# Kernel optimization log

Measured on AMD Instinct MI355X. Metric: run time of the kernel, lower is better.

## Reference

```python
import jax, jax.numpy as jnp
import numpy as np

B, S, DIM = 2, 1024, 2048
H, NOPE, ROPE_D, VD = 16, 128, 64, 128
QKD = NOPE + ROPE_D  # 192
BASE = 10000
NEG_INF = -1e9


def _rope_cos_sin(seq_len, start_pos=0):
    # theta: [ROPE_D//2]
    theta = 1.0 / (BASE ** (jnp.arange(0, ROPE_D, 2, dtype=jnp.float32) / ROPE_D))
    pos = jnp.arange(start_pos, start_pos + seq_len, dtype=jnp.float32)
    ang = pos[:, None] * theta[None, :]  # [s, ROPE_D//2]
    return jnp.cos(ang), jnp.sin(ang)


def _apply_rope(x, cos, sin):
    # x: [b, s, h, d]; cos/sin: [s, d//2]
    b, s, h, d = x.shape
    xs = x.astype(jnp.float32).reshape(b, s, h, d // 2, 2)
    c = cos[None, :, None, :]
    sn = sin[None, :, None, :]
    out = jnp.stack([xs[..., 0] * c - xs[..., 1] * sn,
                     xs[..., 1] * c + xs[..., 0] * sn], axis=-1)
    return out.reshape(b, s, h, d).astype(x.dtype)


def setup_inputs() -> dict:
    key = jax.random.key(0)
    ks = jax.random.split(key, 6)
    x = jax.random.normal(ks[0], (B, S, DIM), dtype=jnp.float32)
    sc = lambda fan_in: 1.0 / np.sqrt(fan_in)
    Wq = jax.random.normal(ks[1], (DIM, H * QKD), dtype=jnp.float32) * sc(DIM)
    Wk = jax.random.normal(ks[2], (DIM, H * QKD), dtype=jnp.float32) * sc(DIM)
    Wv = jax.random.normal(ks[3], (DIM, H * VD), dtype=jnp.float32) * sc(DIM)
    Wo = jax.random.normal(ks[4], (H * VD, DIM), dtype=jnp.float32) * sc(H * VD)
    bo = jnp.zeros((DIM,), dtype=jnp.float32)
    mask = jnp.where(jnp.tril(jnp.ones((S, S), dtype=bool)), 0.0, NEG_INF).astype(jnp.float32)
    return {"x": x, "Wq": Wq, "Wk": Wk, "Wv": Wv, "Wo": Wo, "bo": bo,
            "mask": mask, "start_pos": 0}


def reference(x, Wq, Wk, Wv, Wo, bo, mask, start_pos):
    b, s, _ = x.shape
    q = (x @ Wq).reshape(b, s, H, QKD)
    k = (x @ Wk).reshape(b, s, H, QKD)
    v = (x @ Wv).reshape(b, s, H, VD)
    q_nope, q_rope = q[..., :NOPE], q[..., NOPE:]
    k_nope, k_rope = k[..., :NOPE], k[..., NOPE:]
    cos, sin = _rope_cos_sin(s)  # input_pos=None -> positions 0..s-1
    q_rope = _apply_rope(q_rope, cos, sin)
    k_rope = _apply_rope(k_rope, cos, sin)
    q = jnp.concatenate([q_nope, q_rope], axis=-1)
    k = jnp.concatenate([k_nope, k_rope], axis=-1)
    # start_pos=0 prefill: cache[:end_pos] == k, v just written
    scale = QKD ** -0.5
    scores = jnp.einsum('bshd,bthd->bsht', q, k) * scale
    scores = scores + mask[:, None, :]  # mask.unsqueeze(1) on [b,s,h,t] broadcasting
    weights = jax.nn.softmax(scores.astype(jnp.float32), axis=-1).astype(x.dtype)
    c_v = jnp.einsum('bsht,bthd->bshd', weights, v)
    return c_v.reshape(b, s, H * VD) @ Wo + bo
```

## Files before the change

kernel.cpp:

```cpp
#include <hip/hip_runtime.h>


typedef __bf16 bf16;
typedef __bf16 bf16x8 __attribute__((ext_vector_type(8)));
typedef __bf16 bf16x4 __attribute__((ext_vector_type(4)));
typedef float  f32x4  __attribute__((ext_vector_type(4)));

#define DEVI __device__ __forceinline__

static constexpr int Bc = 2, Sc = 1024, DIMc = 2048, Hc = 16;
static constexpr int NOPEc = 128, QKDc = 192, VDc = 128;
static constexpr int NQ    = Hc * QKDc;
static constexpr int NCAT  = NQ + NQ + Hc*VDc;

__global__ __launch_bounds__(256) void k_prep(const float* __restrict__ x,
                                              const float* __restrict__ Wq, const float* __restrict__ Wk,
                                              const float* __restrict__ Wv, const float* __restrict__ Wo,
                                              bf16* __restrict__ xb, bf16* __restrict__ wcat,
                                              bf16* __restrict__ woT,
                                              float* __restrict__ cosT, float* __restrict__ sinT) {
    __shared__ float tile[64][68];
    const int yt = blockIdx.y, xt = blockIdx.x, tid = threadIdx.x;
    if (yt < 160) {
        const float* src; bf16* dst; int N, n0;
        if (yt < 48)       { src = Wq; N = 3072; n0 = yt * 64;         dst = wcat; }
        else if (yt < 96)  { src = Wk; N = 3072; n0 = (yt - 48) * 64;  dst = wcat + (size_t)3072 * 2048; }
        else if (yt < 128) { src = Wv; N = 2048; n0 = (yt - 96) * 64;  dst = wcat + (size_t)6144 * 2048; }
        else               { src = Wo; N = 2048; n0 = (yt - 128) * 64; dst = woT; }
        int k0 = xt * 64;
        int tr = tid >> 4, tc = (tid & 15) * 4;
#pragma unroll
        for (int i = 0; i < 4; i++) {
            int r = tr + i * 16;
            float4 v = *(const float4*)(src + (size_t)(k0 + r) * N + n0 + tc);
            tile[r][tc+0] = v.x; tile[r][tc+1] = v.y; tile[r][tc+2] = v.z; tile[r][tc+3] = v.w;
        }
        __syncthreads();
#pragma unroll
        for (int i = 0; i < 4; i++) {
            int n = tr + i * 16;
            bf16x4 o;
#pragma unroll
            for (int j = 0; j < 4; j++) o[j] = (bf16)tile[tc + j][n];
            *(bf16x4*)(dst + (size_t)(n0 + n) * 2048 + k0 + tc) = o;
        }
    } else if (yt < 224) {
        int i = (((yt - 160) * 32 + xt) * 256 + tid) * 8;
        float4 a = *(const float4*)(x + i);
        float4 b = *(const float4*)(x + i + 4);
        bf16x8 o;
        o[0]=(bf16)a.x; o[1]=(bf16)a.y; o[2]=(bf16)a.z; o[3]=(bf16)a.w;
        o[4]=(bf16)b.x; o[5]=(bf16)b.y; o[6]=(bf16)b.z; o[7]=(bf16)b.w;
        *(bf16x8*)(xb + i) = o;
    } else {
#pragma unroll
        for (int p = 0; p < 4; p++) {
            int idx = p * 8192 + xt * 256 + tid;
            int pos = idx >> 5, i = idx & 31;
            float theta = expf(-(float)i * (9.210340371976184f / 32.0f));
            float ang = (float)pos * theta;
            cosT[idx] = cosf(ang);
            sinT[idx] = sinf(ang);
        }
    }
}

__global__ __launch_bounds__(256) void k_rope2(bf16* __restrict__ qkv, const float* __restrict__ cosT,
                                               const float* __restrict__ sinT) {
    int bidx = blockIdx.x;
    int secbase = (bidx >= 1024) ? NQ : 0;
    int idx = (bidx & 1023) * 256 + threadIdx.x;
    int g = idx & 7, h = (idx >> 3) & 15, row = idx >> 7;
    int s = row & (Sc - 1);
    bf16* p = qkv + (size_t)row * NCAT + secbase + h * QKDc + NOPEc + g * 8;
    bf16x8 v = *(bf16x8*)p;
    const float* cp = cosT + s * 32 + g * 4;
    const float* sp = sinT + s * 32 + g * 4;
#pragma unroll
    for (int q = 0; q < 4; q++) {
        float x0 = (float)v[2*q], x1 = (float)v[2*q+1];
        float c = cp[q], sn = sp[q];
        v[2*q]   = (bf16)(x0 * c - x1 * sn);
        v[2*q+1] = (bf16)(x1 * c + x0 * sn);
    }
    *(bf16x8*)p = v;
}

__global__ __launch_bounds__(256) void k_vt(const bf16* __restrict__ qkv, bf16* __restrict__ vT) {
    int st = blockIdx.x, dt = blockIdx.y, bh = blockIdx.z;
    int b = bh >> 4, h = bh & 15;
    __shared__ bf16 tile[64][72];
    int r = threadIdx.x >> 3, c8 = (threadIdx.x & 7) * 8;
    const bf16* src = qkv + (size_t)(b * Sc + st * 64) * NCAT + 2 * NQ + h * VDc + dt * 64;
#pragma unroll
    for (int i = 0; i < 2; i++) {
        int rr = r + i * 32;
        *(bf16x8*)&tile[rr][c8] = *(const bf16x8*)(src + (size_t)rr * NCAT + c8);
    }
    __syncthreads();
    bf16* dst = vT + ((size_t)bh * 128 + dt * 64) * Sc + st * 64;
#pragma unroll
    for (int i = 0; i < 2; i++) {
        int rr = r + i * 32;
        bf16x8 o;
#pragma unroll
        for (int j = 0; j < 8; j++) o[j] = tile[c8 + j][rr];
        *(bf16x8*)(dst + (size_t)rr * Sc + c8) = o;
    }
}

DEVI void gload16(const bf16* g, bf16* l) {
    __builtin_amdgcn_global_load_lds((const __attribute__((address_space(1))) void*)g,
                                     (__attribute__((address_space(3))) void*)l, 16, 0, 0);
}

__global__ __launch_bounds__(512, 2) void k_gemm8(const bf16* __restrict__ A, const bf16* __restrict__ Bt,
                                                  bf16* __restrict__ C, int N, int K, int NCT) {
    __shared__ __align__(16) bf16 lds[2][2][2][256 * 32];
    const int tid = threadIdx.x;
    const int l = tid & 63, wid = tid >> 6;
    const int lg = l >> 4, lc = l & 15;
    const int wm = wid >> 2, wn = wid & 3;
    const int bid = blockIdx.x;
    const int xcd = bid & 7, g = bid >> 3;
    const int per = NCT >> 3;
    const int rt = g & 7, ct = xcd * per + (g >> 3);
    const int row0 = rt * 256, col0 = ct * 256;
    const int NT = K >> 6;

    const bf16* Abase = A  + (size_t)row0 * K;
    const bf16* Bbase = Bt + (size_t)col0 * K;

    size_t srcoff0, srcoff1;
    int ldsoff0, ldsoff1;
    {
        int li0 = tid,        r0 = li0 >> 2, u0 = li0 & 3;
        int li1 = 512 + tid,  r1 = li1 >> 2, u1 = li1 & 3;
        srcoff0 = (size_t)r0 * K + ((u0 ^ ((r0 >> 1) & 3)) << 3);  ldsoff0 = li0 * 8;
        srcoff1 = (size_t)r1 * K + ((u1 ^ ((r1 >> 1) & 3)) << 3);  ldsoff1 = li1 * 8;
    }

#define STAGE8(ab, ks, ktile, buf) { \
    const bf16* gb_ = ((ab) ? Bbase : Abase) + (ktile) * 64 + (ks) * 32; \
    bf16* lb_ = &lds[buf][ab][ks][0]; \
    gload16(gb_ + srcoff0, lb_ + ldsoff0); \
    gload16(gb_ + srcoff1, lb_ + ldsoff1); }

    f32x4 acc[8][4] = {};

    STAGE8(0, 0, 0, 0); STAGE8(1, 0, 0, 0); STAGE8(0, 1, 0, 0); STAGE8(1, 1, 0, 0);
    asm volatile("s_waitcnt vmcnt(4)" ::: "memory");
    __builtin_amdgcn_s_barrier();
    asm volatile("" ::: "memory");

    for (int kt = 0; kt < NT; ++kt) {
        const int cur = kt & 1, nxt = cur ^ 1;
        const bool notlast = (kt + 1 < NT);
        bf16x8 aF[4], bB[4];
#pragma unroll
        for (int ph = 0; ph < 4; ph++) {
            const int ks = ph >> 1, mh = ph & 1;
            const bf16* As_ = &lds[cur][0][ks][0];
            const bf16* Bs_ = &lds[cur][1][ks][0];
            if (mh == 0) {
#pragma unroll
                for (int fc = 0; fc < 4; fc++) {
                    int row = wn * 64 + fc * 16 + lc;
                    bB[fc] = *(const bf16x8*)(Bs_ + row * 32 + ((lg ^ ((row >> 1) & 3)) << 3));
                }
            }
#pragma unroll
            for (int i = 0; i < 4; i++) {
                int row = wm * 128 + (mh * 4 + i) * 16 + lc;
                aF[i] = *(const bf16x8*)(As_ + row * 32 + ((lg ^ ((row >> 1) & 3)) << 3));
            }
            if (notlast) {
                if      (ph == 0) STAGE8(0, 0, kt + 1, nxt)
                else if (ph == 1) STAGE8(1, 0, kt + 1, nxt)
                else if (ph == 2) STAGE8(0, 1, kt + 1, nxt)
                else              STAGE8(1, 1, kt + 1, nxt)
            }
            __builtin_amdgcn_s_barrier();
            asm volatile("" ::: "memory");
            __builtin_amdgcn_s_setprio(1);
#pragma unroll
            for (int i = 0; i < 4; i++)
#pragma unroll
                for (int fc = 0; fc < 4; fc++)
                    acc[mh * 4 + i][fc] =
                        __builtin_amdgcn_mfma_f32_16x16x32_bf16(aF[i], bB[fc], acc[mh * 4 + i][fc], 0, 0, 0);
            __builtin_amdgcn_s_setprio(0);
            if (ph == 1) {
                if (notlast) asm volatile("s_waitcnt vmcnt(4)" ::: "memory");
                else         asm volatile("s_waitcnt vmcnt(0)" ::: "memory");
            }
            if (ph == 3 && notlast) {
                asm volatile("s_waitcnt vmcnt(4)" ::: "memory");
            }
            __builtin_amdgcn_s_barrier();
            asm volatile("" ::: "memory");
        }
    }
#undef STAGE8
#pragma unroll
    for (int m = 0; m < 8; m++)
#pragma unroll
        for (int fc = 0; fc < 4; fc++)
#pragma unroll
            for (int j = 0; j < 4; j++) {
                int r = row0 + wm * 128 + m * 16 + lg * 4 + j;
                int c = col0 + wn * 64 + fc * 16 + lc;
                C[(size_t)r * N + c] = (bf16)acc[m][fc][j];
            }
}

__global__ __launch_bounds__(512, 2) void k_gemmO(const bf16* __restrict__ A, const bf16* __restrict__ Bt,
                                                  float* __restrict__ C, const float* __restrict__ bias,
                                                  int N, int K) {
    __shared__ __align__(16) bf16 lds[2][2][2][128 * 32];
    const int tid = threadIdx.x;
    const int l = tid & 63, wid = tid >> 6;
    const int lg = l >> 4, lc = l & 15;
    const int wm = wid >> 2, wn = wid & 3;
    const int bid = blockIdx.x;
    const int xcd = bid & 7, g = bid >> 3;
    const int rt = g & 15, ct = xcd * 2 + (g >> 4);
    const int row0 = rt * 128, col0 = ct * 128;
    const int NT = K >> 6;

    const bf16* Abase = A  + (size_t)row0 * K;
    const bf16* Bbase = Bt + (size_t)col0 * K;

    size_t srcoff; int ldsoff;
    {
        int r0 = tid >> 2, u0 = tid & 3;
        srcoff = (size_t)r0 * K + ((u0 ^ ((r0 >> 1) & 3)) << 3);
        ldsoff = tid * 8;
    }

#define STAGEO(ab, ks, ktile, buf) { \
    const bf16* gb_ = ((ab) ? Bbase : Abase) + (ktile) * 64 + (ks) * 32; \
    gload16(gb_ + srcoff, &lds[buf][ab][ks][0] + ldsoff); }

    f32x4 acc[4][2] = {};

    STAGEO(0, 0, 0, 0); STAGEO(1, 0, 0, 0); STAGEO(0, 1, 0, 0); STAGEO(1, 1, 0, 0);
    asm volatile("s_waitcnt vmcnt(2)" ::: "memory");
    __builtin_amdgcn_s_barrier();
    asm volatile("" ::: "memory");

    for (int kt = 0; kt < NT; ++kt) {
        const int cur = kt & 1, nxt = cur ^ 1;
        const bool notlast = (kt + 1 < NT);
#pragma unroll
        for (int ph = 0; ph < 2; ph++) {
            const bf16* As_ = &lds[cur][0][ph][0];
            const bf16* Bs_ = &lds[cur][1][ph][0];
            bf16x8 aF[4], bB[2];
#pragma unroll
            for (int n = 0; n < 2; n++) {
                int row = wn * 32 + n * 16 + lc;
                bB[n] = *(const bf16x8*)(Bs_ + row * 32 + ((lg ^ ((row >> 1) & 3)) << 3));
            }
#pragma unroll
            for (int m = 0; m < 4; m++) {
                int row = wm * 64 + m * 16 + lc;
                aF[m] = *(const bf16x8*)(As_ + row * 32 + ((lg ^ ((row >> 1) & 3)) << 3));
            }
            if (notlast) {
                if (ph == 0) { STAGEO(0, 0, kt + 1, nxt); STAGEO(1, 0, kt + 1, nxt); }
                else         { STAGEO(0, 1, kt + 1, nxt); STAGEO(1, 1, kt + 1, nxt); }
            }
            __builtin_amdgcn_s_barrier();
            asm volatile("" ::: "memory");
            __builtin_amdgcn_s_setprio(1);
#pragma unroll
            for (int m = 0; m < 4; m++)
#pragma unroll
                for (int n = 0; n < 2; n++)
                    acc[m][n] = __builtin_amdgcn_mfma_f32_16x16x32_bf16(aF[m], bB[n], acc[m][n], 0, 0, 0);
            __builtin_amdgcn_s_setprio(0);
            if (notlast)          asm volatile("s_waitcnt vmcnt(2)" ::: "memory");
            else if (ph == 0)     asm volatile("s_waitcnt vmcnt(0)" ::: "memory");
            __builtin_amdgcn_s_barrier();
            asm volatile("" ::: "memory");
        }
    }
#undef STAGEO
#pragma unroll
    for (int m = 0; m < 4; m++)
#pragma unroll
        for (int n = 0; n < 2; n++)
#pragma unroll
            for (int j = 0; j < 4; j++) {
                int r = row0 + wm * 64 + m * 16 + lg * 4 + j;
                int c = col0 + wn * 32 + n * 16 + lc;
                C[(size_t)r * N + c] = acc[m][n][j] + bias[c];
            }
}

__global__ __launch_bounds__(256, 3) void k_attn(const bf16* __restrict__ qkv, const bf16* __restrict__ vT,
                                                 bf16* __restrict__ cv) {
    const int bid = blockIdx.x;
    const int xcd = bid & 7, g = bid >> 3;
    const int qt = (g & 32) ? (g & 15) : (15 - (g & 15));
    const int bh = xcd + 8 * (g >> 4);
    const int b = bh >> 4, h = bh & 15;
    const int tid = threadIdx.x, l = tid & 63, w = tid >> 6;
    const int lg = l >> 4, lc = l & 15;
    __shared__ __align__(16) bf16 Ks[64 * 192];
    __shared__ __align__(16) bf16 Vs[128 * 64];
    __shared__ __align__(16) bf16 Pl[4][16][72];
    const bf16* Qb = qkv + (size_t)b * Sc * NCAT + h * QKDc;
    const bf16* Kb = Qb + NQ;
    const bf16* Vt = vT + (size_t)bh * 128 * Sc;

    int sK[6];
#pragma unroll
    for (int r = 0; r < 6; r++) {
        int li = r * 256 + tid;
        int row = li / 24, c16 = li - row * 24;
        sK[r] = row * NCAT + ((c16 ^ (row & 7)) * 8);
    }
    int sV[4];
#pragma unroll
    for (int r = 0; r < 4; r++) {
        int li = r * 256 + tid;
        int row = li >> 3, c16 = li & 7;
        sV[r] = row * Sc + ((c16 ^ (row & 7)) * 8);
    }
    const int swz = lc & 7;

    bf16x8 qF[6];
    const int qrow = qt * 64 + w * 16 + lc;
#pragma unroll
    for (int kc = 0; kc < 6; kc++) qF[kc] = *(const bf16x8*)(Qb + (size_t)qrow * NCAT + kc * 32 + lg * 8);

    f32x4 acc[8] = {};
    float mrow[4] = {-1e30f, -1e30f, -1e30f, -1e30f};
    float lsum[4] = {0.f, 0.f, 0.f, 0.f};
    const float scale = 0.07216878364870323f;

#pragma unroll
    for (int r = 0; r < 6; r++) gload16(Kb + sK[r], Ks + (r * 256 + tid) * 8);

    for (int c = 0; c <= qt; ++c) {
        const int t0 = c * 64;
        __syncthreads();
#pragma unroll
        for (int r = 0; r < 4; r++) gload16(Vt + t0 + sV[r], Vs + (r * 256 + tid) * 8);
        f32x4 sc[4] = {};
#pragma unroll
        for (int nt = 0; nt < 4; nt++)
#pragma unroll
            for (int kc = 0; kc < 6; kc++) {
                bf16x8 kf = *(const bf16x8*)(Ks + (nt * 16 + lc) * 192 + (((kc * 4 + lg) ^ swz) * 8));
                sc[nt] = __builtin_amdgcn_mfma_f32_16x16x32_bf16(qF[kc], kf, sc[nt], 0, 0, 0);
            }
        __syncthreads();
        if (c < qt) {
#pragma unroll
            for (int r = 0; r < 6; r++) gload16(Kb + (size_t)(t0 + 64) * NCAT + sK[r], Ks + (r * 256 + tid) * 8);
        }
        float p[4][4];
        float cmax[4] = {-1e30f, -1e30f, -1e30f, -1e30f};
        const bool diag = (c == qt);
#pragma unroll
        for (int nt = 0; nt < 4; nt++)
#pragma unroll
            for (int j = 0; j < 4; j++) {
                float v = sc[nt][j] * scale;
                if (diag) {
                    int tg = t0 + nt * 16 + lc;
                    int rg = qt * 64 + w * 16 + lg * 4 + j;
                    if (tg > rg) v = -1e9f;
                }
                p[nt][j] = v;
                cmax[j] = fmaxf(cmax[j], v);
            }
#pragma unroll
        for (int j = 0; j < 4; j++)
#pragma unroll
            for (int d = 1; d < 16; d <<= 1) cmax[j] = fmaxf(cmax[j], __shfl_xor(cmax[j], d));
        float f[4];
#pragma unroll
        for (int j = 0; j < 4; j++) {
            float nm = fmaxf(mrow[j], cmax[j]);
            f[j] = __expf(mrow[j] - nm);
            mrow[j] = nm;
        }
        float psum[4] = {0.f, 0.f, 0.f, 0.f};
#pragma unroll
        for (int nt = 0; nt < 4; nt++)
#pragma unroll
            for (int j = 0; j < 4; j++) {
                p[nt][j] = __expf(p[nt][j] - mrow[j]);
                psum[j] += p[nt][j];
            }
#pragma unroll
        for (int j = 0; j < 4; j++) {
#pragma unroll
            for (int d = 1; d < 16; d <<= 1) psum[j] += __shfl_xor(psum[j], d);
            lsum[j] = lsum[j] * f[j] + psum[j];
        }
#pragma unroll
        for (int n = 0; n < 8; n++)
#pragma unroll
            for (int j = 0; j < 4; j++) acc[n][j] *= f[j];
#pragma unroll
        for (int nt = 0; nt < 4; nt++)
#pragma unroll
            for (int j = 0; j < 4; j++)
                Pl[w][lg * 4 + j][nt * 16 + lc] = (bf16)p[nt][j];
#pragma unroll
        for (int ks = 0; ks < 2; ks++) {
            bf16x8 aP = *(const bf16x8*)(&Pl[w][lc][ks * 32 + lg * 8]);
#pragma unroll
            for (int n = 0; n < 8; n++) {
                bf16x8 bV = *(const bf16x8*)(Vs + (n * 16 + lc) * 64 + (((ks * 4 + lg) ^ swz) * 8));
                acc[n] = __builtin_amdgcn_mfma_f32_16x16x32_bf16(aP, bV, acc[n], 0, 0, 0);
            }
        }
    }
#pragma unroll
    for (int j = 0; j < 4; j++) {
        float inv = 1.0f / lsum[j];
        int r = qt * 64 + w * 16 + lg * 4 + j;
#pragma unroll
        for (int n = 0; n < 8; n++) {
            float v = acc[n][j] * inv;
            cv[((size_t)(b * Sc + r) * Hc + h) * VDc + n * 16 + lc] = (bf16)v;
        }
    }
}

extern "C" void kernel_launch(void* const* d_in, const int* in_sizes, int n_in,
                              void* d_out, int out_size, void* d_ws, size_t ws_size,
                              hipStream_t stream) {
    const float* x  = (const float*)d_in[0];
    const float* Wq = (const float*)d_in[1];
    const float* Wk = (const float*)d_in[2];
    const float* Wv = (const float*)d_in[3];
    const float* Wo = (const float*)d_in[4];
    const float* bo = (const float*)d_in[5];
    float* out = (float*)d_out;
    char* ws = (char*)d_ws;

    bf16*  wcat = (bf16*)(ws + 0);
    bf16*  woT  = (bf16*)(ws + 33554432);
    bf16*  xb   = (bf16*)(ws + 41943040);
    bf16*  qkvb = (bf16*)(ws + 50331648);
    bf16*  cvb  = (bf16*)(ws + 83886080);
    bf16*  vTb  = (bf16*)(ws + 92274688);
    float* cosT = (float*)(ws + 100663296);
    float* sinT = (float*)(ws + 100794368);

    k_prep<<<dim3(32, 225), 256, 0, stream>>>(x, Wq, Wk, Wv, Wo, xb, wcat, woT, cosT, sinT);
    k_gemm8<<<256, 512, 0, stream>>>(xb, wcat, qkvb, NCAT, DIMc, NCAT / 256);
    k_rope2<<<2048, 256, 0, stream>>>(qkvb, cosT, sinT);
    k_vt<<<dim3(16, 2, 32), 256, 0, stream>>>(qkvb, vTb);
    k_attn<<<512, 256, 0, stream>>>(qkvb, vTb, cvb);
    k_gemmO<<<256, 512, 0, stream>>>(cvb, woT, out, bo, DIMc, DIMc);
}
```

Before: 163.9 us.

## Software-pipeline LDS fragment reads ahead of MFMA phases in QKV GEMM

Result: no change. 163.9 us (-0.0%).

```diff
diff --git a/kernel.cpp b/kernel.cpp
--- a/kernel.cpp
+++ b/kernel.cpp
@@ -146,62 +146,73 @@
     gload16(gb_ + srcoff0, lb_ + ldsoff0); \
     gload16(gb_ + srcoff1, lb_ + ldsoff1); }
 
+#define RD_A(dst, P, hf) { _Pragma("unroll") \
+    for (int i_ = 0; i_ < 4; i_++) { \
+        int row_ = wm * 128 + ((hf) * 4 + i_) * 16 + lc; \
+        dst[i_] = *(const bf16x8*)((P) + row_ * 32 + ((lg ^ ((row_ >> 1) & 3)) << 3)); } }
+#define RD_B(dst, P) { _Pragma("unroll") \
+    for (int fc_ = 0; fc_ < 4; fc_++) { \
+        int row_ = wn * 64 + fc_ * 16 + lc; \
+        dst[fc_] = *(const bf16x8*)((P) + row_ * 32 + ((lg ^ ((row_ >> 1) & 3)) << 3)); } }
+#define MM(Av, Bv, mo) { _Pragma("unroll") \
+    for (int i_ = 0; i_ < 4; i_++) _Pragma("unroll") \
+        for (int fc_ = 0; fc_ < 4; fc_++) \
+            acc[(mo) + i_][fc_] = __builtin_amdgcn_mfma_f32_16x16x32_bf16(Av[i_], Bv[fc_], acc[(mo) + i_][fc_], 0, 0, 0); }
+#define BAR() { __builtin_amdgcn_s_barrier(); asm volatile("" ::: "memory"); }
+
     f32x4 acc[8][4] = {};
 
     STAGE8(0, 0, 0, 0); STAGE8(1, 0, 0, 0); STAGE8(0, 1, 0, 0); STAGE8(1, 1, 0, 0);
     asm volatile("s_waitcnt vmcnt(4)" ::: "memory");
-    __builtin_amdgcn_s_barrier();
-    asm volatile("" ::: "memory");
+    BAR();
 
     for (int kt = 0; kt < NT; ++kt) {
         const int cur = kt & 1, nxt = cur ^ 1;
         const bool notlast = (kt + 1 < NT);
-        bf16x8 aF[4], bB[4];
-#pragma unroll
-        for (int ph = 0; ph < 4; ph++) {
-            const int ks = ph >> 1, mh = ph & 1;
-            const bf16* As_ = &lds[cur][0][ks][0];
-            const bf16* Bs_ = &lds[cur][1][ks][0];
-            if (mh == 0) {
-#pragma unroll
-                for (int fc = 0; fc < 4; fc++) {
-                    int row = wn * 64 + fc * 16 + lc;
-                    bB[fc] = *(const bf16x8*)(Bs_ + row * 32 + ((lg ^ ((row >> 1) & 3)) << 3));
-                }
-            }
-#pragma unroll
-            for (int i = 0; i < 4; i++) {
-                int row = wm * 128 + (mh * 4 + i) * 16 + lc;
-                aF[i] = *(const bf16x8*)(As_ + row * 32 + ((lg ^ ((row >> 1) & 3)) << 3));
-            }
-            if (notlast) {
-                if      (ph == 0) STAGE8(0, 0, kt + 1, nxt)
-                else if (ph == 1) STAGE8(1, 0, kt + 1, nxt)
-                else if (ph == 2) STAGE8(0, 1, kt + 1, nxt)
-                else              STAGE8(1, 1, kt + 1, nxt)
-            }
-            __builtin_amdgcn_s_barrier();
-            asm volatile("" ::: "memory");
-            __builtin_amdgcn_s_setprio(1);
-#pragma unroll
-            for (int i = 0; i < 4; i++)
-#pragma unroll
-                for (int fc = 0; fc < 4; fc++)
-                    acc[mh * 4 + i][fc] =
-                        __builtin_amdgcn_mfma_f32_16x16x32_bf16(aF[i], bB[fc], acc[mh * 4 + i][fc], 0, 0, 0);
-            __builtin_amdgcn_s_setprio(0);
-            if (ph == 1) {
-                if (notlast) asm volatile("s_waitcnt vmcnt(4)" ::: "memory");
-                else         asm volatile("s_waitcnt vmcnt(0)" ::: "memory");
-            }
-            if (ph == 3 && notlast) {
-                asm volatile("s_waitcnt vmcnt(4)" ::: "memory");
-            }
-            __builtin_amdgcn_s_barrier();
-            asm volatile("" ::: "memory");
-        }
+        const bf16* A0_ = &lds[cur][0][0][0];
+        const bf16* A1_ = &lds[cur][0][1][0];
+        const bf16* B0_ = &lds[cur][1][0][0];
+        const bf16* B1_ = &lds[cur][1][1][0];
+        bf16x8 aX[4], aY[4], bX[4], bY[4];
+        RD_A(aX, A0_, 0);
+        RD_B(bX, B0_);
+        if (notlast) STAGE8(0, 0, kt + 1, nxt);
+        RD_A(aY, A0_, 1);
+        BAR();
+        __builtin_amdgcn_s_setprio(1);
+        MM(aX, bX, 0);
+        __builtin_amdgcn_s_setprio(0);
+        if (notlast) asm volatile("s_waitcnt vmcnt(2)" ::: "memory");
+        else         asm volatile("s_waitcnt vmcnt(0)" ::: "memory");
+        BAR();
+        if (notlast) STAGE8(1, 0, kt + 1, nxt);
+        RD_A(aX, A1_, 0);
+        RD_B(bY, B1_);
+        BAR();
+        __builtin_amdgcn_s_setprio(1);
+        MM(aY, bX, 4);
+        __builtin_amdgcn_s_setprio(0);
+        BAR();
+        if (notlast) STAGE8(0, 1, kt + 1, nxt);
+        RD_A(aY, A1_, 1);
+        BAR();
+        __builtin_amdgcn_s_setprio(1);
+        MM(aX, bY, 0);
+        __builtin_amdgcn_s_setprio(0);
+        BAR();
+        if (notlast) STAGE8(1, 1, kt + 1, nxt);
+        BAR();
+        __builtin_amdgcn_s_setprio(1);
+        MM(aY, bY, 4);
+        __builtin_amdgcn_s_setprio(0);
+        if (notlast) asm volatile("s_waitcnt vmcnt(4)" ::: "memory");
+        BAR();
     }
 #undef STAGE8
+#undef RD_A
+#undef RD_B
+#undef MM
+#undef BAR
 #pragma unroll
     for (int m = 0; m < 8; m++)
 #pragma unroll
```

## Shrink QKV GEMM tile to 256x128 with single-phase K=32 loop; fuse rope and V-transpose

Applied to the files above, without the earlier changes.

Measured after the change: 166.9 us. About the same (+1.8%).

```diff
diff --git a/kernel.cpp b/kernel.cpp
--- a/kernel.cpp
+++ b/kernel.cpp
@@ -65,47 +65,48 @@
     }
 }
 
-__global__ __launch_bounds__(256) void k_rope2(bf16* __restrict__ qkv, const float* __restrict__ cosT,
-                                               const float* __restrict__ sinT) {
-    int bidx = blockIdx.x;
-    int secbase = (bidx >= 1024) ? NQ : 0;
-    int idx = (bidx & 1023) * 256 + threadIdx.x;
-    int g = idx & 7, h = (idx >> 3) & 15, row = idx >> 7;
-    int s = row & (Sc - 1);
-    bf16* p = qkv + (size_t)row * NCAT + secbase + h * QKDc + NOPEc + g * 8;
-    bf16x8 v = *(bf16x8*)p;
-    const float* cp = cosT + s * 32 + g * 4;
-    const float* sp = sinT + s * 32 + g * 4;
-#pragma unroll
-    for (int q = 0; q < 4; q++) {
-        float x0 = (float)v[2*q], x1 = (float)v[2*q+1];
-        float c = cp[q], sn = sp[q];
-        v[2*q]   = (bf16)(x0 * c - x1 * sn);
-        v[2*q+1] = (bf16)(x1 * c + x0 * sn);
-    }
-    *(bf16x8*)p = v;
-}
-
-__global__ __launch_bounds__(256) void k_vt(const bf16* __restrict__ qkv, bf16* __restrict__ vT) {
-    int st = blockIdx.x, dt = blockIdx.y, bh = blockIdx.z;
-    int b = bh >> 4, h = bh & 15;
-    __shared__ bf16 tile[64][72];
-    int r = threadIdx.x >> 3, c8 = (threadIdx.x & 7) * 8;
-    const bf16* src = qkv + (size_t)(b * Sc + st * 64) * NCAT + 2 * NQ + h * VDc + dt * 64;
-#pragma unroll
-    for (int i = 0; i < 2; i++) {
-        int rr = r + i * 32;
-        *(bf16x8*)&tile[rr][c8] = *(const bf16x8*)(src + (size_t)rr * NCAT + c8);
-    }
-    __syncthreads();
-    bf16* dst = vT + ((size_t)bh * 128 + dt * 64) * Sc + st * 64;
-#pragma unroll
-    for (int i = 0; i < 2; i++) {
-        int rr = r + i * 32;
-        bf16x8 o;
-#pragma unroll
-        for (int j = 0; j < 8; j++) o[j] = tile[c8 + j][rr];
-        *(bf16x8*)(dst + (size_t)rr * Sc + c8) = o;
+__global__ __launch_bounds__(256) void k_ropevt(bf16* __restrict__ qkv, const float* __restrict__ cosT,
+                                                const float* __restrict__ sinT, bf16* __restrict__ vT) {
+    const int bidx = blockIdx.x, tid = threadIdx.x;
+    if (bidx < 2048) {
+        int secbase = (bidx >= 1024) ? NQ : 0;
+        int idx = (bidx & 1023) * 256 + tid;
+        int g = idx & 7, h = (idx >> 3) & 15, row = idx >> 7;
+        int s = row & (Sc - 1);
+        bf16* p = qkv + (size_t)row * NCAT + secbase + h * QKDc + NOPEc + g * 8;
+        bf16x8 v = *(bf16x8*)p;
+        const float* cp = cosT + s * 32 + g * 4;
+        const float* sp = sinT + s * 32 + g * 4;
+#pragma unroll
+        for (int q = 0; q < 4; q++) {
+            float x0 = (float)v[2*q], x1 = (float)v[2*q+1];
+            float c = cp[q], sn = sp[q];
+            v[2*q]   = (bf16)(x0 * c - x1 * sn);
+            v[2*q+1] = (bf16)(x1 * c + x0 * sn);
+        }
+        *(bf16x8*)p = v;
+    } else {
+        __shared__ bf16 tile[64][72];
+        const int vb = bidx - 2048;
+        const int st = vb & 15, dt = (vb >> 4) & 1, bh = vb >> 5;
+        const int b = bh >> 4, h = bh & 15;
+        int r = tid >> 3, c8 = (tid & 7) * 8;
+        const bf16* src = qkv + (size_t)(b * Sc + st * 64) * NCAT + 2 * NQ + h * VDc + dt * 64;
+#pragma unroll
+        for (int i = 0; i < 2; i++) {
+            int rr = r + i * 32;
+            *(bf16x8*)&tile[rr][c8] = *(const bf16x8*)(src + (size_t)rr * NCAT + c8);
+        }
+        __syncthreads();
+        bf16* dst = vT + ((size_t)bh * 128 + dt * 64) * Sc + st * 64;
+#pragma unroll
+        for (int i = 0; i < 2; i++) {
+            int rr = r + i * 32;
+            bf16x8 o;
+#pragma unroll
+            for (int j = 0; j < 8; j++) o[j] = tile[c8 + j][rr];
+            *(bf16x8*)(dst + (size_t)rr * Sc + c8) = o;
+        }
     }
 }
 
@@ -114,101 +115,84 @@
                                      (__attribute__((address_space(3))) void*)l, 16, 0, 0);
 }
 
-__global__ __launch_bounds__(512, 2) void k_gemm8(const bf16* __restrict__ A, const bf16* __restrict__ Bt,
-                                                  bf16* __restrict__ C, int N, int K, int NCT) {
-    __shared__ __align__(16) bf16 lds[2][2][2][256 * 32];
+__global__ __launch_bounds__(512, 4) void k_gemm8(const bf16* __restrict__ A, const bf16* __restrict__ Bt,
+                                                  bf16* __restrict__ C, int N, int K) {
+    __shared__ __align__(16) bf16 lds[2][12288];
     const int tid = threadIdx.x;
     const int l = tid & 63, wid = tid >> 6;
     const int lg = l >> 4, lc = l & 15;
-    const int wm = wid >> 2, wn = wid & 3;
+    const int wm = wid >> 1, wn = wid & 1;
     const int bid = blockIdx.x;
     const int xcd = bid & 7, g = bid >> 3;
-    const int per = NCT >> 3;
-    const int rt = g & 7, ct = xcd * per + (g >> 3);
-    const int row0 = rt * 256, col0 = ct * 256;
-    const int NT = K >> 6;
+    const int rt = g & 7, ct = xcd * 8 + (g >> 3);
+    const int row0 = rt * 256, col0 = ct * 128;
+    const int NT = K >> 5;
 
     const bf16* Abase = A  + (size_t)row0 * K;
     const bf16* Bbase = Bt + (size_t)col0 * K;
 
-    size_t srcoff0, srcoff1;
-    int ldsoff0, ldsoff1;
+    size_t srcA0, srcA1, srcB0;
+    int ldsA0, ldsA1, ldsB0;
     {
-        int li0 = tid,        r0 = li0 >> 2, u0 = li0 & 3;
-        int li1 = 512 + tid,  r1 = li1 >> 2, u1 = li1 & 3;
-        srcoff0 = (size_t)r0 * K + ((u0 ^ ((r0 >> 1) & 3)) << 3);  ldsoff0 = li0 * 8;
-        srcoff1 = (size_t)r1 * K + ((u1 ^ ((r1 >> 1) & 3)) << 3);  ldsoff1 = li1 * 8;
-    }
-
-#define STAGE8(ab, ks, ktile, buf) { \
-    const bf16* gb_ = ((ab) ? Bbase : Abase) + (ktile) * 64 + (ks) * 32; \
-    bf16* lb_ = &lds[buf][ab][ks][0]; \
-    gload16(gb_ + srcoff0, lb_ + ldsoff0); \
-    gload16(gb_ + srcoff1, lb_ + ldsoff1); }
-
-    f32x4 acc[8][4] = {};
-
-    STAGE8(0, 0, 0, 0); STAGE8(1, 0, 0, 0); STAGE8(0, 1, 0, 0); STAGE8(1, 1, 0, 0);
-    asm volatile("s_waitcnt vmcnt(4)" ::: "memory");
+        int r0 = tid >> 2,        u0 = tid & 3;
+        int r1 = (512+tid) >> 2,  u1 = tid & 3;
+        srcA0 = (size_t)r0 * K + ((u0 ^ ((r0 >> 1) & 3)) << 3);  ldsA0 = tid * 8;
+        srcA1 = (size_t)r1 * K + ((u1 ^ ((r1 >> 1) & 3)) << 3);  ldsA1 = (512 + tid) * 8;
+        srcB0 = (size_t)r0 * K + ((u0 ^ ((r0 >> 1) & 3)) << 3);  ldsB0 = 8192 + tid * 8;
+    }
+
+#define STAGE(ktile, buf) { \
+    const bf16* ga_ = Abase + (ktile) * 32; \
+    const bf16* gb_ = Bbase + (ktile) * 32; \
+    gload16(ga_ + srcA0, &lds[buf][0] + ldsA0); \
+    gload16(ga_ + srcA1, &lds[buf][0] + ldsA1); \
+    gload16(gb_ + srcB0, &lds[buf][0] + ldsB0); }
+
+    f32x4 acc[4][4] = {};
+
+    STAGE(0, 0);
+    asm volatile("s_waitcnt vmcnt(0)" ::: "memory");
     __builtin_amdgcn_s_barrier();
     asm volatile("" ::: "memory");
 
     for (int kt = 0; kt < NT; ++kt) {
         const int cur = kt & 1, nxt = cur ^ 1;
         const bool notlast = (kt + 1 < NT);
+        if (notlast) STAGE(kt + 1, nxt);
+        const bf16* As_ = &lds[cur][0];
+        const bf16* Bs_ = &lds[cur][8192];
         bf16x8 aF[4], bB[4];
 #pragma unroll
-        for (int ph = 0; ph < 4; ph++) {
-            const int ks = ph >> 1, mh = ph & 1;
-            const bf16* As_ = &lds[cur][0][ks][0];
-            const bf16* Bs_ = &lds[cur][1][ks][0];
-            if (mh == 0) {
-#pragma unroll
-                for (int fc = 0; fc < 4; fc++) {
-                    int row = wn * 64 + fc * 16 + lc;
-                    bB[fc] = *(const bf16x8*)(Bs_ + row * 32 + ((lg ^ ((row >> 1) & 3)) << 3));
-                }
-            }
-#pragma unroll
-            for (int i = 0; i < 4; i++) {
-                int row = wm * 128 + (mh * 4 + i) * 16 + lc;
-                aF[i] = *(const bf16x8*)(As_ + row * 32 + ((lg ^ ((row >> 1) & 3)) << 3));
-            }
-            if (notlast) {
-                if      (ph == 0) STAGE8(0, 0, kt + 1, nxt)
-                else if (ph == 1) STAGE8(1, 0, kt + 1, nxt)
-                else if (ph == 2) STAGE8(0, 1, kt + 1, nxt)
-                else              STAGE8(1, 1, kt + 1, nxt)
-            }
+        for (int i = 0; i < 4; i++) {
+            int row = wm * 64 + i * 16 + lc;
+            aF[i] = *(const bf16x8*)(As_ + row * 32 + ((lg ^ ((row >> 1) & 3)) << 3));
+        }
+#pragma unroll
+        for (int fc = 0; fc < 4; fc++) {
+            int row = wn * 64 + fc * 16 + lc;
+            bB[fc] = *(const bf16x8*)(Bs_ + row * 32 + ((lg ^ ((row >> 1) & 3)) << 3));
+        }
+        __builtin_amdgcn_s_setprio(1);
+#pragma unroll
+        for (int i = 0; i < 4; i++)
+#pragma unroll
+            for (int fc = 0; fc < 4; fc++)
+                acc[i][fc] = __builtin_amdgcn_mfma_f32_16x16x32_bf16(aF[i], bB[fc], acc[i][fc], 0, 0, 0);
+        __builtin_amdgcn_s_setprio(0);
+        if (notlast) {
+            asm volatile("s_waitcnt vmcnt(0)" ::: "memory");
             __builtin_amdgcn_s_barrier();
             asm volatile("" ::: "memory");
-            __builtin_amdgcn_s_setprio(1);
-#pragma unroll
-            for (int i = 0; i < 4; i++)
-#pragma unroll
-                for (int fc = 0; fc < 4; fc++)
-                    acc[mh * 4 + i][fc] =
-                        __builtin_amdgcn_mfma_f32_16x16x32_bf16(aF[i], bB[fc], acc[mh * 4 + i][fc], 0, 0, 0);
-            __builtin_amdgcn_s_setprio(0);
-            if (ph == 1) {
-                if (notlast) asm volatile("s_waitcnt vmcnt(4)" ::: "memory");
-                else         asm volatile("s_waitcnt vmcnt(0)" ::: "memory");
-            }
-            if (ph == 3 && notlast) {
-                asm volatile("s_waitcnt vmcnt(4)" ::: "memory");
-            }
-            __builtin_amdgcn_s_barrier();
-            asm volatile("" ::: "memory");
-        }
-    }
-#undef STAGE8
-#pragma unroll
-    for (int m = 0; m < 8; m++)
+        }
+    }
+#undef STAGE
+#pragma unroll
+    for (int m = 0; m < 4; m++)
 #pragma unroll
         for (int fc = 0; fc < 4; fc++)
 #pragma unroll
             for (int j = 0; j < 4; j++) {
-                int r = row0 + wm * 128 + m * 16 + lg * 4 + j;
+                int r = row0 + wm * 64 + m * 16 + lg * 4 + j;
                 int c = col0 + wn * 64 + fc * 16 + lc;
                 C[(size_t)r * N + c] = (bf16)acc[m][fc][j];
             }
@@ -456,9 +440,8 @@
     float* sinT = (float*)(ws + 100794368);
 
     k_prep<<<dim3(32, 225), 256, 0, stream>>>(x, Wq, Wk, Wv, Wo, xb, wcat, woT, cosT, sinT);
-    k_gemm8<<<256, 512, 0, stream>>>(xb, wcat, qkvb, NCAT, DIMc, NCAT / 256);
-    k_rope2<<<2048, 256, 0, stream>>>(qkvb, cosT, sinT);
-    k_vt<<<dim3(16, 2, 32), 256, 0, stream>>>(qkvb, vTb);
+    k_gemm8<<<512, 512, 0, stream>>>(xb, wcat, qkvb, NCAT, DIMc);
+    k_ropevt<<<3072, 256, 0, stream>>>(qkvb, cosT, sinT, vTb);
     k_attn<<<512, 256, 0, stream>>>(qkvb, vTb, cvb);
     k_gemmO<<<256, 512, 0, stream>>>(cvb, woT, out, bo, DIMc, DIMc);
 }
```
